# Performance work log

Hardware: AMD Instinct MI355X
Metric: run time of the kernel (lower is better)

Reference implementation:

```python
import jax, jax.numpy as jnp
import numpy as np

B, C, W, H, NH, FF, L = 4, 200, 300, 128, 8, 512, 2
PH = H // NH
MAXLEN = 200
PE_N = 512
NEG = -1e15


def _sinusoidal_pe():
    # fairseq-style sinusoidal table, get_embedding(512, hidden_size)
    half = H // 2
    freq = np.exp(np.arange(half, dtype=np.float64) * -(np.log(10000.0) / (half - 1)))
    ang = np.arange(PE_N, dtype=np.float64)[:, None] * freq[None, :]
    return jnp.asarray(np.concatenate([np.sin(ang), np.cos(ang)], axis=1), jnp.float32)

PE = _sinusoidal_pe()  # [512, H], frozen (requires_grad=False in torch)


def setup_inputs() -> dict:
    key = jax.random.key(0)
    ks = jax.random.split(key, 20)

    def lin(k, fan_in, shape):
        lim = 1.0 / np.sqrt(fan_in)
        return jax.random.uniform(k, shape, jnp.float32, -lim, lim)

    return {
        'chars': jax.random.normal(ks[0], (B, C, H), jnp.float32),
        'words': jax.random.normal(ks[1], (B, W, H), jnp.float32),
        'pos_s': jax.random.randint(ks[2], (B, C), 0, MAXLEN),
        'pos_e': jax.random.randint(ks[3], (B, C), 0, MAXLEN),
        'lex_s': jax.random.randint(ks[4], (B, W), 0, MAXLEN),
        'lex_e': jax.random.randint(ks[5], (B, W), 0, MAXLEN),
        'seq_len': jax.random.randint(ks[6], (B,), 100, C + 1),
        'lex_num': jax.random.randint(ks[7], (B,), 150, W + 1),
        # Four_Pos_Fusion 'ff': Linear(4H -> H) + ReLU
        'Wf': lin(ks[8], 4 * H, (4 * H, H)),
        'bf': jnp.zeros((H,), jnp.float32),
        # per-layer attention / FFN params, stacked on leading layer dim
        'Wq': lin(ks[9], H, (L, H, H)),  'bq': jnp.zeros((L, H), jnp.float32),
        'Wk': lin(ks[10], H, (L, H, H)), 'bk': jnp.zeros((L, H), jnp.float32),
        'Wv': lin(ks[11], H, (L, H, H)), 'bv': jnp.zeros((L, H), jnp.float32),
        'Wr': lin(ks[12], H, (L, H, H)), 'br': jnp.zeros((L, H), jnp.float32),
        'u_bias': jax.random.normal(ks[13], (L, NH, PH), jnp.float32) * 0.02,
        'v_bias': jax.random.normal(ks[14], (L, NH, PH), jnp.float32) * 0.02,
        'ln1_g': jnp.ones((L, H), jnp.float32), 'ln1_b': jnp.zeros((L, H), jnp.float32),
        'ln2_g': jnp.ones((L, H), jnp.float32), 'ln2_b': jnp.zeros((L, H), jnp.float32),
        'W1': lin(ks[15], H, (L, H, FF)),  'b1': jnp.zeros((L, FF), jnp.float32),
        'W2': lin(ks[16], FF, (L, FF, H)), 'b2': jnp.zeros((L, H), jnp.float32),
    }


def _ln(x, g, b):
    m = jnp.mean(x, -1, keepdims=True)
    v = jnp.var(x, -1, keepdims=True)
    return (x - m) / jnp.sqrt(v + 1e-5) * g + b


def reference(chars, words, pos_s, pos_e, lex_s, lex_e, seq_len, lex_num,
              Wf, bf, Wq, bq, Wk, bk, Wv, bv, Wr, br, u_bias, v_bias,
              ln1_g, ln1_b, ln2_g, ln2_b, W1, b1, W2, b2):
    # four relative-position distance tables (char span vs word span), offset by max_seq_len
    idx = lambda p, l: jnp.clip(p[:, :, None] - l[:, None, :] + MAXLEN, 0, PE_N - 1)
    # Linear(4H->H) over the concat of four gathered PE tensors, expressed as
    # a sum of 4 chunked matmuls to avoid materializing the [B,C,W,4H] concat.
    rel = (PE[idx(pos_s, lex_s)] @ Wf[0:H] + PE[idx(pos_s, lex_e)] @ Wf[H:2 * H]
           + PE[idx(pos_e, lex_s)] @ Wf[2 * H:3 * H] + PE[idx(pos_e, lex_e)] @ Wf[3 * H:4 * H] + bf)
    rel = jax.nn.relu(rel)  # [B, C, W, H]

    # char_lex_len_to_mask: valid (char i, word j) pairs
    mask = (jnp.arange(C) < seq_len[:, None])[:, :, None] & (jnp.arange(W) < lex_num[:, None])[:, None, :]
    mask = mask[:, None]  # [B, 1, C, W]

    out = chars
    for i in range(L):
        q = (out @ Wq[i] + bq[i]).reshape(B, C, NH, PH)
        k = (words @ Wk[i] + bk[i]).reshape(B, W, NH, PH)
        v = (words @ Wv[i] + bv[i]).reshape(B, W, NH, PH)
        r = (rel @ Wr[i] + br[i]).reshape(B, C, W, NH, PH)
        A_C = jnp.einsum('bcnp,bwnp->bncw', q + u_bias[i], k)
        B_D = jnp.einsum('bcnp,bcwnp->bncw', q + v_bias[i], r)
        score = jnp.where(mask, A_C + B_D, NEG)  # scale=False
        att = jax.nn.softmax(score, axis=-1)
        att = jnp.where(mask, att, 0.0)  # dropout=0 (eval)
        ctx = jnp.einsum('bncw,bwnp->bcnp', att, v).reshape(B, C, H)
        out = _ln(ctx + out, ln1_g[i], ln1_b[i])
        ff = jax.nn.relu(out @ W1[i] + b1[i]) @ W2[i] + b2[i]
        out = _ln(ff + out, ln2_g[i], ln2_b[i])
    return out
```

## Files before the change

kernel.cpp:

```cpp
#include <hip/hip_runtime.h>
#include <math.h>

#define B_ 4
#define C_ 200
#define CH_ 100
#define W_ 300
#define WP_ 304
#define H_ 128
#define NH_ 8
#define PH_ 16
#define FF_ 512
#define L_ 2
#define MAXLEN_ 200
#define PEN_ 512
#define WVS_ 136

typedef __bf16 bf16x8 __attribute__((ext_vector_type(8)));
typedef float f32x4v __attribute__((ext_vector_type(4)));

#define SEG_PEW   512
#define SEG_KV    (SEG_PEW + B_ * W_)
#define SEG_WR    (SEG_KV + 256)
#define SEG_W1T   (SEG_WR + 128)
#define PREP_BLOCKS (SEG_W1T + 128)

__global__ __launch_bounds__(128) void prep_kernel(
        const float* __restrict__ Wf, const float* __restrict__ bfv,
        const float* __restrict__ words,
        const float* __restrict__ Wk, const float* __restrict__ bk,
        const float* __restrict__ Wv, const float* __restrict__ bv,
        const float* __restrict__ Wr, const float* __restrict__ W1,
        const float* __restrict__ W2,
        __bf16* __restrict__ kb, __bf16* __restrict__ PEWb, __bf16* __restrict__ vTb,
        __bf16* __restrict__ WrB, __bf16* __restrict__ W1T, __bf16* __restrict__ W2T) {
    __shared__ __align__(16) float s_row[H_];
    __shared__ float s_tile[32][33];
    int t = threadIdx.x;
    if (blockIdx.x < SEG_PEW) {
        int p = blockIdx.x;
        {
            int j = (t < 64) ? t : (t - 64);
            double f = exp(-(double)j * (log(10000.0) / 63.0));
            double a = (double)p * f;
            s_row[t] = (float)((t < 64) ? sin(a) : cos(a));
        }
        __syncthreads();
        float acc0 = 0.f, acc1 = 0.f, acc2 = 0.f, acc3 = 0.f;
        for (int j = 0; j < H_; ++j) {
            float xv = s_row[j];
            int row = j * H_ + t;
            acc0 += xv * Wf[0 * H_ * H_ + row];
            acc1 += xv * Wf[1 * H_ * H_ + row];
            acc2 += xv * Wf[2 * H_ * H_ + row];
            acc3 += xv * Wf[3 * H_ * H_ + row];
        }
        PEWb[(0 * PEN_ + p) * H_ + t] = (__bf16)(acc0 + bfv[t]);
        PEWb[(1 * PEN_ + p) * H_ + t] = (__bf16)acc1;
        PEWb[(2 * PEN_ + p) * H_ + t] = (__bf16)acc2;
        PEWb[(3 * PEN_ + p) * H_ + t] = (__bf16)acc3;
    } else if (blockIdx.x < SEG_KV) {
        int rem = blockIdx.x - SEG_PEW;
        int bb = rem / W_, w = rem % W_;
        s_row[t] = words[rem * H_ + t];
        __syncthreads();
        const float4* row4 = (const float4*)s_row;
        #pragma unroll 1
        for (int li = 0; li < L_; ++li) {
            const float* wk = Wk + li * H_ * H_;
            const float* wv = Wv + li * H_ * H_;
            float4 ak = {0,0,0,0}, av = {0,0,0,0};
            #pragma unroll 2
            for (int g = 0; g < 32; ++g) {
                float4 x = row4[g];
                int j0 = 4 * g;
                ak.x += x.x * wk[(j0 + 0) * H_ + t];
                ak.y += x.y * wk[(j0 + 1) * H_ + t];
                ak.z += x.z * wk[(j0 + 2) * H_ + t];
                ak.w += x.w * wk[(j0 + 3) * H_ + t];
                av.x += x.x * wv[(j0 + 0) * H_ + t];
                av.y += x.y * wv[(j0 + 1) * H_ + t];
                av.z += x.z * wv[(j0 + 2) * H_ + t];
                av.w += x.w * wv[(j0 + 3) * H_ + t];
            }
            kb[(size_t)(li * B_ * W_ + rem) * H_ + t] =
                (__bf16)((ak.x + ak.y) + (ak.z + ak.w) + bk[li * H_ + t]);
            size_t vrow = ((size_t)(li * B_ + bb) * H_ + t) * WP_;
            vTb[vrow + w] = (__bf16)((av.x + av.y) + (av.z + av.w) + bv[li * H_ + t]);
            if (w == 0) {
                vTb[vrow + 300] = (__bf16)0.f; vTb[vrow + 301] = (__bf16)0.f;
                vTb[vrow + 302] = (__bf16)0.f; vTb[vrow + 303] = (__bf16)0.f;
            }
        }
    } else if (blockIdx.x < SEG_WR) {
        int i = (blockIdx.x - SEG_KV) * 128 + t;
        WrB[i] = (__bf16)Wr[i];
    } else if (blockIdx.x < SEG_W1T) {
        int blk = blockIdx.x - SEG_WR;
        int l = blk >> 6;
        int rem = blk & 63;
        int jt = rem >> 4;
        int ut = rem & 15;
        int r = t >> 5, cc = t & 31;
        #pragma unroll
        for (int k = 0; k < 8; ++k) {
            int j = jt * 32 + r + 4 * k;
            s_tile[r + 4 * k][cc] = W1[(l * H_ + j) * FF_ + ut * 32 + cc];
        }
        __syncthreads();
        int jl = t & 31, ul = t >> 5;
        #pragma unroll
        for (int k = 0; k < 8; ++k) {
            int u = ut * 32 + ul + 4 * k;
            W1T[((size_t)(l * FF_ + u)) * H_ + jt * 32 + jl] = (__bf16)s_tile[jl][ul + 4 * k];
        }
    } else {
        int blk = blockIdx.x - SEG_W1T;
        int l = blk >> 6;
        int rem = blk & 63;
        int ut = rem >> 2;
        int ht = rem & 3;
        int r = t >> 5, cc = t & 31;
        #pragma unroll
        for (int k = 0; k < 8; ++k) {
            int u = ut * 32 + r + 4 * k;
            s_tile[r + 4 * k][cc] = W2[(l * FF_ + u) * H_ + ht * 32 + cc];
        }
        __syncthreads();
        int ul = t & 31, hl = t >> 5;
        #pragma unroll
        for (int k = 0; k < 8; ++k) {
            int h = ht * 32 + hl + 4 * k;
            W2T[((size_t)(l * H_ + h)) * FF_ + ut * 32 + ul] = (__bf16)s_tile[ul][hl + 4 * k];
        }
    }
}

__global__ __launch_bounds__(256, 2) void mega_kernel(
    const float* __restrict__ chars,
    const int* __restrict__ pos_s, const int* __restrict__ pos_e,
    const int* __restrict__ lex_s, const int* __restrict__ lex_e,
    const int* __restrict__ seq_len, const int* __restrict__ lex_num,
    const float* __restrict__ Wq, const float* __restrict__ bq,
    const float* __restrict__ br,
    const float* __restrict__ u_bias, const float* __restrict__ v_bias,
    const float* __restrict__ ln1_g, const float* __restrict__ ln1_b,
    const float* __restrict__ ln2_g, const float* __restrict__ ln2_b,
    const float* __restrict__ b1, const float* __restrict__ b2,
    const __bf16* __restrict__ kb, const __bf16* __restrict__ PEWb,
    const __bf16* __restrict__ vTb, const __bf16* __restrict__ WrB,
    const __bf16* __restrict__ W1T, const __bf16* __restrict__ W2T,
    float* __restrict__ out) {

    __shared__ __align__(16) float s_x[2][H_], s_qv[2][H_];
    __shared__ __align__(16) __bf16 s_wvecb[2][16][WVS_];
    __shared__ __align__(16) __bf16 s_qub[2][16][WVS_];
    __shared__ float s_bterm[2][NH_];
    __shared__ __align__(16) float s_sc[2][NH_][WP_];
    __shared__ float s_red[2][132];
    __shared__ __align__(16) float s_hid[2][FF_];
    __shared__ float s_tmp[2][256];
    __shared__ int s_ls[W_], s_le[W_];

    int blk = blockIdx.x;
    int b = blk / CH_, c0 = blk % CH_;
    int t = threadIdx.x;
    int lane = t & 63;
    int wid = t >> 6;
    int l15 = lane & 15, quad = lane >> 4;

    if (t < H_) {
        s_x[0][t] = chars[(b * C_ + c0) * H_ + t];
        s_x[1][t] = chars[(b * C_ + c0 + CH_) * H_ + t];
    }
    for (int w = t; w < W_; w += 256) {
        s_ls[w] = lex_s[b * W_ + w];
        s_le[w] = lex_e[b * W_ + w];
    }
    for (int i = t; i < 2 * 8 * WVS_; i += 256) {
        int r = i / (8 * WVS_), rem = i % (8 * WVS_);
        s_wvecb[r][8 + rem / WVS_][rem % WVS_] = (__bf16)0.f;
    }
    for (int i = t; i < 2 * 16 * WVS_; i += 256) {
        int r = i / (16 * WVS_), rem = i % (16 * WVS_);
        s_qub[r][rem / WVS_][rem % WVS_] = (__bf16)0.f;
    }
    int ps0 = pos_s[b * C_ + c0],        pev0 = pos_e[b * C_ + c0];
    int ps1 = pos_s[b * C_ + c0 + CH_],  pev1 = pos_e[b * C_ + c0 + CH_];
    int slen = seq_len[b];
    int cvalid0 = (c0 < slen), cvalid1 = (c0 + CH_ < slen);
    int wnum = lex_num[b];
    __syncthreads();

    for (int li = 0; li < L_; ++li) {
        {
            int half = t >> 7, h = t & 127;
            const float* WqL = Wq + li * H_ * H_;
            const float4* x40 = (const float4*)s_x[0];
            const float4* x41 = (const float4*)s_x[1];
            float4 a0 = {0,0,0,0}, a1 = {0,0,0,0};
            #pragma unroll 2
            for (int g = half * 16; g < half * 16 + 16; ++g) {
                float4 xa = x40[g], xb = x41[g];
                int j0 = 4 * g;
                float w0 = WqL[(j0 + 0) * H_ + h], w1 = WqL[(j0 + 1) * H_ + h];
                float w2 = WqL[(j0 + 2) * H_ + h], w3 = WqL[(j0 + 3) * H_ + h];
                a0.x += xa.x * w0; a0.y += xa.y * w1; a0.z += xa.z * w2; a0.w += xa.w * w3;
                a1.x += xb.x * w0; a1.y += xb.y * w1; a1.z += xb.z * w2; a1.w += xb.w * w3;
            }
            s_tmp[0][t] = (a0.x + a0.y) + (a0.z + a0.w);
            s_tmp[1][t] = (a1.x + a1.y) + (a1.z + a1.w);
        }
        __syncthreads();
        if (t < H_) {
            #pragma unroll
            for (int r = 0; r < 2; ++r) {
                float acc = s_tmp[r][t] + s_tmp[r][t + 128] + bq[li * H_ + t];
                s_qub[r][t >> 4][t] = (__bf16)(acc + u_bias[li * H_ + t]);
                s_qv[r][t] = acc + v_bias[li * H_ + t];
            }
        }
        __syncthreads();

        if (t < H_) {
            const __bf16* WrRow = WrB + li * H_ * H_ + t * H_;
            #pragma unroll 2
            for (int n = 0; n < NH_; ++n) {
                bf16x8 w0 = *(const bf16x8*)(WrRow + n * PH_);
                bf16x8 w1 = *(const bf16x8*)(WrRow + n * PH_ + 8);
                #pragma unroll
                for (int r = 0; r < 2; ++r) {
                    const float4* qv4 = (const float4*)(s_qv[r] + n * PH_);
                    float4 q0 = qv4[0], q1 = qv4[1], q2 = qv4[2], q3 = qv4[3];
                    float4 a4;
                    a4.x = (float)w0[0] * q0.x + (float)w1[0] * q2.x;
                    a4.y = (float)w0[1] * q0.y + (float)w1[1] * q2.y;
                    a4.z = (float)w0[2] * q0.z + (float)w1[2] * q2.z;
                    a4.w = (float)w0[3] * q0.w + (float)w1[3] * q2.w;
                    a4.x += (float)w0[4] * q1.x + (float)w1[4] * q3.x;
                    a4.y += (float)w0[5] * q1.y + (float)w1[5] * q3.y;
                    a4.z += (float)w0[6] * q1.z + (float)w1[6] * q3.z;
                    a4.w += (float)w0[7] * q1.w + (float)w1[7] * q3.w;
                    s_wvecb[r][n][t] = (__bf16)((a4.x + a4.y) + (a4.z + a4.w));
                }
            }
        } else if (t < H_ + NH_) {
            int n = t - H_;
            const float4* br4 = (const float4*)(br + li * H_ + n * PH_);
            float4 b0 = br4[0], b1v = br4[1], b2v = br4[2], b3v = br4[3];
            #pragma unroll
            for (int r = 0; r < 2; ++r) {
                const float4* qv4 = (const float4*)(s_qv[r] + n * PH_);
                float4 q0 = qv4[0], q1 = qv4[1], q2 = qv4[2], q3 = qv4[3];
                float4 a4;
                a4.x = b0.x * q0.x + b2v.x * q2.x;
                a4.y = b0.y * q0.y + b2v.y * q2.y;
                a4.z = b0.z * q0.z + b2v.z * q2.z;
                a4.w = b0.w * q0.w + b2v.w * q2.w;
                a4.x += b1v.x * q1.x + b3v.x * q3.x;
                a4.y += b1v.y * q1.y + b3v.y * q3.y;
                a4.z += b1v.z * q1.z + b3v.z * q3.z;
                a4.w += b1v.w * q1.w + b3v.w * q3.w;
                s_bterm[r][n] = (a4.x + a4.y) + (a4.z + a4.w);
            }
        }
        __syncthreads();

        const __bf16* kL = kb + (size_t)(li * B_ + b) * W_ * H_;
        for (int tile = wid; tile < (W_ + 15) / 16; tile += 4) {
            int w0t = tile * 16;
            int w = w0t + l15; if (w > W_ - 1) w = W_ - 1;
            int ls = s_ls[w], le = s_le[w];
            int i00 = min(max(ps0 - ls + MAXLEN_, 0), PEN_ - 1);
            int i01 = min(max(ps0 - le + MAXLEN_, 0), PEN_ - 1);
            int i02 = min(max(pev0 - ls + MAXLEN_, 0), PEN_ - 1);
            int i03 = min(max(pev0 - le + MAXLEN_, 0), PEN_ - 1);
            int i10 = min(max(ps1 - ls + MAXLEN_, 0), PEN_ - 1);
            int i11 = min(max(ps1 - le + MAXLEN_, 0), PEN_ - 1);
            int i12 = min(max(pev1 - ls + MAXLEN_, 0), PEN_ - 1);
            int i13 = min(max(pev1 - le + MAXLEN_, 0), PEN_ - 1);
            const __bf16* r00 = PEWb + (size_t)(0 * PEN_ + i00) * H_;
            const __bf16* r01 = PEWb + (size_t)(1 * PEN_ + i01) * H_;
            const __bf16* r02 = PEWb + (size_t)(2 * PEN_ + i02) * H_;
            const __bf16* r03 = PEWb + (size_t)(3 * PEN_ + i03) * H_;
            const __bf16* r10 = PEWb + (size_t)(0 * PEN_ + i10) * H_;
            const __bf16* r11 = PEWb + (size_t)(1 * PEN_ + i11) * H_;
            const __bf16* r12 = PEWb + (size_t)(2 * PEN_ + i12) * H_;
            const __bf16* r13 = PEWb + (size_t)(3 * PEN_ + i13) * H_;
            const __bf16* kr = kL + (size_t)w * H_;
            const __bf16* wrow0 = &s_wvecb[0][l15][0];
            const __bf16* wrow1 = &s_wvecb[1][l15][0];
            const __bf16* qrow0 = &s_qub[0][l15][0];
            const __bf16* qrow1 = &s_qub[1][l15][0];
            f32x4v acc0 = {0.f,0.f,0.f,0.f}, acc1 = {0.f,0.f,0.f,0.f};
            #pragma unroll 1
            for (int s = 0; s < 4; ++s) {
                int h0 = s * 32 + quad * 8;
                bf16x8 K = *(const bf16x8*)(kr + h0);
                {
                    bf16x8 t0 = *(const bf16x8*)(r00 + h0);
                    bf16x8 t1 = *(const bf16x8*)(r01 + h0);
                    bf16x8 t2 = *(const bf16x8*)(r02 + h0);
                    bf16x8 t3 = *(const bf16x8*)(r03 + h0);
                    bf16x8 A;
                    #pragma unroll
                    for (int j = 0; j < 8; ++j)
                        A[j] = (__bf16)fmaxf((float)t0[j] + (float)t1[j] + (float)t2[j] + (float)t3[j], 0.f);
                    bf16x8 Bf = *(const bf16x8*)(wrow0 + h0);
                    acc0 = __builtin_amdgcn_mfma_f32_16x16x32_bf16(A, Bf, acc0, 0, 0, 0);
                    bf16x8 Bq = *(const bf16x8*)(qrow0 + h0);
                    acc0 = __builtin_amdgcn_mfma_f32_16x16x32_bf16(K, Bq, acc0, 0, 0, 0);
                }
                {
                    bf16x8 t0 = *(const bf16x8*)(r10 + h0);
                    bf16x8 t1 = *(const bf16x8*)(r11 + h0);
                    bf16x8 t2 = *(const bf16x8*)(r12 + h0);
                    bf16x8 t3 = *(const bf16x8*)(r13 + h0);
                    bf16x8 A;
                    #pragma unroll
                    for (int j = 0; j < 8; ++j)
                        A[j] = (__bf16)fmaxf((float)t0[j] + (float)t1[j] + (float)t2[j] + (float)t3[j], 0.f);
                    bf16x8 Bf = *(const bf16x8*)(wrow1 + h0);
                    acc1 = __builtin_amdgcn_mfma_f32_16x16x32_bf16(A, Bf, acc1, 0, 0, 0);
                    bf16x8 Bq = *(const bf16x8*)(qrow1 + h0);
                    acc1 = __builtin_amdgcn_mfma_f32_16x16x32_bf16(K, Bq, acc1, 0, 0, 0);
                }
            }
            if (l15 < NH_) {
                float bt0 = s_bterm[0][l15], bt1 = s_bterm[1][l15];
                #pragma unroll
                for (int r = 0; r < 4; ++r) {
                    int wr = w0t + quad * 4 + r;
                    if (wr < W_) {
                        s_sc[0][l15][wr] = acc0[r] + bt0;
                        s_sc[1][l15][wr] = acc1[r] + bt1;
                    }
                }
            }
        }
        __syncthreads();

        {
            int n = t >> 5, ln_ = t & 31;
            #pragma unroll
            for (int r = 0; r < 2; ++r) {
                int cval = r ? cvalid1 : cvalid0;
                if (cval) {
                    float m = -INFINITY;
                    for (int w = ln_; w < wnum; w += 32) m = fmaxf(m, s_sc[r][n][w]);
                    #pragma unroll
                    for (int off = 16; off > 0; off >>= 1) m = fmaxf(m, __shfl_xor(m, off, 32));
                    float sum = 0.f;
                    for (int w = ln_; w < wnum; w += 32) sum += expf(s_sc[r][n][w] - m);
                    #pragma unroll
                    for (int off = 16; off > 0; off >>= 1) sum += __shfl_xor(sum, off, 32);
                    float inv = 1.f / sum;
                    for (int w = ln_; w < WP_; w += 32)
                        s_sc[r][n][w] = (w < wnum) ? expf(s_sc[r][n][w] - m) * inv : 0.f;
                } else {
                    for (int w = ln_; w < WP_; w += 32) s_sc[r][n][w] = 0.f;
                }
            }
        }
        __syncthreads();

        {
            int h = t & 127, half = t >> 7, n = h >> 4;
            const __bf16* vrow = vTb + ((size_t)(li * B_ + b) * H_ + h) * WP_;
            const float4* att0 = (const float4*)(s_sc[0][n]);
            const float4* att1 = (const float4*)(s_sc[1][n]);
            float4 a0 = {0,0,0,0}, a1 = {0,0,0,0};
            #pragma unroll 2
            for (int g = half * 19; g < half * 19 + 19; ++g) {
                bf16x8 vv = *(const bf16x8*)(vrow + 8 * g);
                float4 p00 = att0[2 * g], p01 = att0[2 * g + 1];
                float4 p10 = att1[2 * g], p11 = att1[2 * g + 1];
                float v0 = (float)vv[0], v1 = (float)vv[1], v2 = (float)vv[2], v3 = (float)vv[3];
                float v4 = (float)vv[4], v5 = (float)vv[5], v6 = (float)vv[6], v7 = (float)vv[7];
                a0.x += p00.x * v0 + p01.x * v4;
                a0.y += p00.y * v1 + p01.y * v5;
                a0.z += p00.z * v2 + p01.z * v6;
                a0.w += p00.w * v3 + p01.w * v7;
                a1.x += p10.x * v0 + p11.x * v4;
                a1.y += p10.y * v1 + p11.y * v5;
                a1.z += p10.z * v2 + p11.z * v6;
                a1.w += p10.w * v3 + p11.w * v7;
            }
            s_tmp[0][t] = (a0.x + a0.y) + (a0.z + a0.w);
            s_tmp[1][t] = (a1.x + a1.y) + (a1.z + a1.w);
        }
        __syncthreads();

        if (t < 128) {
            s_red[0][t] = s_tmp[0][t] + s_tmp[0][t + 128] + s_x[0][t];
        } else {
            int e = t - 128;
            s_red[1][e] = s_tmp[1][e] + s_tmp[1][e + 128] + s_x[1][e];
        }
        __syncthreads();
        if (t < 128) {
            int r = t >> 6, l = t & 63;
            float a = s_red[r][l], bb = s_red[r][l + 64];
            float s = a + bb, ss = a * a + bb * bb;
            #pragma unroll
            for (int off = 32; off > 0; off >>= 1) {
                s += __shfl_down(s, off);
                ss += __shfl_down(ss, off);
            }
            if (l == 0) {
                float mean = s * (1.f / 128.f);
                float var = ss * (1.f / 128.f) - mean * mean;
                s_red[r][128] = mean;
                s_red[r][129] = rsqrtf(var + 1e-5f);
            }
        }
        __syncthreads();
        if (t < H_) {
            float g1 = ln1_g[li * H_ + t], b1v = ln1_b[li * H_ + t];
            #pragma unroll
            for (int r = 0; r < 2; ++r)
                s_x[r][t] = (s_red[r][t] - s_red[r][128]) * s_red[r][129] * g1 + b1v;
        }
        __syncthreads();

        {
            const __bf16* W1l = W1T + (size_t)li * FF_ * H_;
            int u0 = t * 2;
            const __bf16* ra = W1l + (size_t)u0 * H_;
            const __bf16* rb = W1l + (size_t)(u0 + 1) * H_;
            const float4* x40 = (const float4*)s_x[0];
            const float4* x41 = (const float4*)s_x[1];
            float4 a00 = {0,0,0,0}, a01 = {0,0,0,0}, a10 = {0,0,0,0}, a11 = {0,0,0,0};
            #pragma unroll 2
            for (int g = 0; g < 16; ++g) {
                bf16x8 wa = *(const bf16x8*)(ra + 8 * g);
                bf16x8 wb = *(const bf16x8*)(rb + 8 * g);
                float4 xa0 = x40[2 * g], xa1 = x40[2 * g + 1];
                float4 xb0 = x41[2 * g], xb1 = x41[2 * g + 1];
                a00.x += xa0.x * (float)wa[0] + xa1.x * (float)wa[4];
                a00.y += xa0.y * (float)wa[1] + xa1.y * (float)wa[5];
                a00.z += xa0.z * (float)wa[2] + xa1.z * (float)wa[6];
                a00.w += xa0.w * (float)wa[3] + xa1.w * (float)wa[7];
                a01.x += xa0.x * (float)wb[0] + xa1.x * (float)wb[4];
                a01.y += xa0.y * (float)wb[1] + xa1.y * (float)wb[5];
                a01.z += xa0.z * (float)wb[2] + xa1.z * (float)wb[6];
                a01.w += xa0.w * (float)wb[3] + xa1.w * (float)wb[7];
                a10.x += xb0.x * (float)wa[0] + xb1.x * (float)wa[4];
                a10.y += xb0.y * (float)wa[1] + xb1.y * (float)wa[5];
                a10.z += xb0.z * (float)wa[2] + xb1.z * (float)wa[6];
                a10.w += xb0.w * (float)wa[3] + xb1.w * (float)wa[7];
                a11.x += xb0.x * (float)wb[0] + xb1.x * (float)wb[4];
                a11.y += xb0.y * (float)wb[1] + xb1.y * (float)wb[5];
                a11.z += xb0.z * (float)wb[2] + xb1.z * (float)wb[6];
                a11.w += xb0.w * (float)wb[3] + xb1.w * (float)wb[7];
            }
            float bb0 = b1[li * FF_ + u0], bb1 = b1[li * FF_ + u0 + 1];
            s_hid[0][u0]     = fmaxf((a00.x + a00.y) + (a00.z + a00.w) + bb0, 0.f);
            s_hid[0][u0 + 1] = fmaxf((a01.x + a01.y) + (a01.z + a01.w) + bb1, 0.f);
            s_hid[1][u0]     = fmaxf((a10.x + a10.y) + (a10.z + a10.w) + bb0, 0.f);
            s_hid[1][u0 + 1] = fmaxf((a11.x + a11.y) + (a11.z + a11.w) + bb1, 0.f);
        }
        __syncthreads();

        {
            int half = t >> 7, h = t & 127;
            const __bf16* wrow2 = W2T + ((size_t)li * H_ + h) * FF_ + half * 256;
            const float4* h40 = (const float4*)(s_hid[0] + half * 256);
            const float4* h41 = (const float4*)(s_hid[1] + half * 256);
            float4 a0 = {0,0,0,0}, a1 = {0,0,0,0};
            #pragma unroll 2
            for (int g = 0; g < 32; ++g) {
                bf16x8 wv = *(const bf16x8*)(wrow2 + 8 * g);
                float4 p00 = h40[2 * g], p01 = h40[2 * g + 1];
                float4 p10 = h41[2 * g], p11 = h41[2 * g + 1];
                float v0 = (float)wv[0], v1 = (float)wv[1], v2 = (float)wv[2], v3 = (float)wv[3];
                float v4 = (float)wv[4], v5 = (float)wv[5], v6 = (float)wv[6], v7 = (float)wv[7];
                a0.x += p00.x * v0 + p01.x * v4;
                a0.y += p00.y * v1 + p01.y * v5;
                a0.z += p00.z * v2 + p01.z * v6;
                a0.w += p00.w * v3 + p01.w * v7;
                a1.x += p10.x * v0 + p11.x * v4;
                a1.y += p10.y * v1 + p11.y * v5;
                a1.z += p10.z * v2 + p11.z * v6;
                a1.w += p10.w * v3 + p11.w * v7;
            }
            s_tmp[0][t] = (a0.x + a0.y) + (a0.z + a0.w);
            s_tmp[1][t] = (a1.x + a1.y) + (a1.z + a1.w);
        }
        __syncthreads();

        if (t < 128) {
            s_red[0][t] = s_tmp[0][t] + s_tmp[0][t + 128] + b2[li * H_ + t] + s_x[0][t];
        } else {
            int e = t - 128;
            s_red[1][e] = s_tmp[1][e] + s_tmp[1][e + 128] + b2[li * H_ + e] + s_x[1][e];
        }
        __syncthreads();
        if (t < 128) {
            int r = t >> 6, l = t & 63;
            float a = s_red[r][l], bb = s_red[r][l + 64];
            float s = a + bb, ss = a * a + bb * bb;
            #pragma unroll
            for (int off = 32; off > 0; off >>= 1) {
                s += __shfl_down(s, off);
                ss += __shfl_down(ss, off);
            }
            if (l == 0) {
                float mean = s * (1.f / 128.f);
                float var = ss * (1.f / 128.f) - mean * mean;
                s_red[r][128] = mean;
                s_red[r][129] = rsqrtf(var + 1e-5f);
            }
        }
        __syncthreads();
        if (t < H_) {
            float g2 = ln2_g[li * H_ + t], b2v = ln2_b[li * H_ + t];
            #pragma unroll
            for (int r = 0; r < 2; ++r)
                s_x[r][t] = (s_red[r][t] - s_red[r][128]) * s_red[r][129] * g2 + b2v;
        }
        __syncthreads();
    }

    if (t < H_) {
        out[(b * C_ + c0) * H_ + t] = s_x[0][t];
        out[(b * C_ + c0 + CH_) * H_ + t] = s_x[1][t];
    }
}

extern "C" void kernel_launch(void* const* d_in, const int* in_sizes, int n_in,
                              void* d_out, int out_size, void* d_ws, size_t ws_size,
                              hipStream_t stream) {
    const float* chars  = (const float*)d_in[0];
    const float* words  = (const float*)d_in[1];
    const int* pos_s   = (const int*)d_in[2];
    const int* pos_e   = (const int*)d_in[3];
    const int* lex_s   = (const int*)d_in[4];
    const int* lex_e   = (const int*)d_in[5];
    const int* seq_len = (const int*)d_in[6];
    const int* lex_num = (const int*)d_in[7];
    const float* Wf  = (const float*)d_in[8];
    const float* bfv = (const float*)d_in[9];
    const float* Wq  = (const float*)d_in[10];
    const float* bq  = (const float*)d_in[11];
    const float* Wk  = (const float*)d_in[12];
    const float* bk  = (const float*)d_in[13];
    const float* Wv  = (const float*)d_in[14];
    const float* bv  = (const float*)d_in[15];
    const float* Wr  = (const float*)d_in[16];
    const float* br  = (const float*)d_in[17];
    const float* u_bias = (const float*)d_in[18];
    const float* v_bias = (const float*)d_in[19];
    const float* ln1_g  = (const float*)d_in[20];
    const float* ln1_b  = (const float*)d_in[21];
    const float* ln2_g  = (const float*)d_in[22];
    const float* ln2_b  = (const float*)d_in[23];
    const float* W1  = (const float*)d_in[24];
    const float* b1  = (const float*)d_in[25];
    const float* W2  = (const float*)d_in[26];
    const float* b2  = (const float*)d_in[27];

    __bf16* kb   = (__bf16*)d_ws;
    __bf16* PEWb = kb + (size_t)L_ * B_ * W_ * H_;
    __bf16* vTb  = PEWb + 4 * PEN_ * H_;
    __bf16* WrB  = vTb + (size_t)L_ * B_ * H_ * WP_;
    __bf16* W1T  = WrB + L_ * H_ * H_;
    __bf16* W2T  = W1T + L_ * H_ * FF_;

    prep_kernel<<<dim3(PREP_BLOCKS), dim3(128), 0, stream>>>(
        Wf, bfv, words, Wk, bk, Wv, bv, Wr, W1, W2,
        kb, PEWb, vTb, WrB, W1T, W2T);

    mega_kernel<<<dim3(B_ * CH_), dim3(256), 0, stream>>>(
        chars, pos_s, pos_e, lex_s, lex_e, seq_len, lex_num,
        Wq, bq, br, u_bias, v_bias,
        ln1_g, ln1_b, ln2_g, ln2_b, b1, b2,
        kb, PEWb, vTb, WrB, W1T, W2T, (float*)d_out);
}
```

Measured before the change: 267.7 us.

## Cache relative-position A fragments in registers across layers

The gathered and ReLU'd positional fusion fragments (A0/A1) are computed once in layer 0 and kept in registers (5x4 bf16x8 per row pair), then reused in layer 1 instead of re-gathering four PE rows and summing again. The layer and tile loops are fully unrolled so the cached arrays can stay in registers. This removes half of the scattered global PE gathers and the conversion arithmetic, but adds up to 160 VGPRs per thread, which risks spills or lower occupancy.

```diff
diff --git a/kernel.cpp b/kernel.cpp
--- a/kernel.cpp
+++ b/kernel.cpp
@@ -14,6 +14,7 @@
 #define MAXLEN_ 200
 #define PEN_ 512
 #define WVS_ 136
+#define NTILE_ 19
 
 typedef __bf16 bf16x8 __attribute__((ext_vector_type(8)));
 typedef float f32x4v __attribute__((ext_vector_type(4)));
@@ -191,6 +192,9 @@
     int wnum = lex_num[b];
     __syncthreads();
 
+    bf16x8 Ac0[5][4], Ac1[5][4];
+
+    #pragma unroll
     for (int li = 0; li < L_; ++li) {
         {
             int half = t >> 7, h = t & 127;
@@ -266,73 +270,98 @@
         __syncthreads();
 
         const __bf16* kL = kb + (size_t)(li * B_ + b) * W_ * H_;
-        for (int tile = wid; tile < (W_ + 15) / 16; tile += 4) {
-            int w0t = tile * 16;
-            int w = w0t + l15; if (w > W_ - 1) w = W_ - 1;
-            int ls = s_ls[w], le = s_le[w];
-            int i00 = min(max(ps0 - ls + MAXLEN_, 0), PEN_ - 1);
-            int i01 = min(max(ps0 - le + MAXLEN_, 0), PEN_ - 1);
-            int i02 = min(max(pev0 - ls + MAXLEN_, 0), PEN_ - 1);
-            int i03 = min(max(pev0 - le + MAXLEN_, 0), PEN_ - 1);
-            int i10 = min(max(ps1 - ls + MAXLEN_, 0), PEN_ - 1);
-            int i11 = min(max(ps1 - le + MAXLEN_, 0), PEN_ - 1);
-            int i12 = min(max(pev1 - ls + MAXLEN_, 0), PEN_ - 1);
-            int i13 = min(max(pev1 - le + MAXLEN_, 0), PEN_ - 1);
-            const __bf16* r00 = PEWb + (size_t)(0 * PEN_ + i00) * H_;
-            const __bf16* r01 = PEWb + (size_t)(1 * PEN_ + i01) * H_;
-            const __bf16* r02 = PEWb + (size_t)(2 * PEN_ + i02) * H_;
-            const __bf16* r03 = PEWb + (size_t)(3 * PEN_ + i03) * H_;
-            const __bf16* r10 = PEWb + (size_t)(0 * PEN_ + i10) * H_;
-            const __bf16* r11 = PEWb + (size_t)(1 * PEN_ + i11) * H_;
-            const __bf16* r12 = PEWb + (size_t)(2 * PEN_ + i12) * H_;
-            const __bf16* r13 = PEWb + (size_t)(3 * PEN_ + i13) * H_;
-            const __bf16* kr = kL + (size_t)w * H_;
+        {
             const __bf16* wrow0 = &s_wvecb[0][l15][0];
             const __bf16* wrow1 = &s_wvecb[1][l15][0];
             const __bf16* qrow0 = &s_qub[0][l15][0];
             const __bf16* qrow1 = &s_qub[1][l15][0];
-            f32x4v acc0 = {0.f,0.f,0.f,0.f}, acc1 = {0.f,0.f,0.f,0.f};
-            #pragma unroll 1
-            for (int s = 0; s < 4; ++s) {
-                int h0 = s * 32 + quad * 8;
-                bf16x8 K = *(const bf16x8*)(kr + h0);
-                {
-                    bf16x8 t0 = *(const bf16x8*)(r00 + h0);
-                    bf16x8 t1 = *(const bf16x8*)(r01 + h0);
-                    bf16x8 t2 = *(const bf16x8*)(r02 + h0);
-                    bf16x8 t3 = *(const bf16x8*)(r03 + h0);
-                    bf16x8 A;
-                    #pragma unroll
-                    for (int j = 0; j < 8; ++j)
-                        A[j] = (__bf16)fmaxf((float)t0[j] + (float)t1[j] + (float)t2[j] + (float)t3[j], 0.f);
-                    bf16x8 Bf = *(const bf16x8*)(wrow0 + h0);
-                    acc0 = __builtin_amdgcn_mfma_f32_16x16x32_bf16(A, Bf, acc0, 0, 0, 0);
-                    bf16x8 Bq = *(const bf16x8*)(qrow0 + h0);
-                    acc0 = __builtin_amdgcn_mfma_f32_16x16x32_bf16(K, Bq, acc0, 0, 0, 0);
-                }
-                {
-                    bf16x8 t0 = *(const bf16x8*)(r10 + h0);
-                    bf16x8 t1 = *(const bf16x8*)(r11 + h0);
-                    bf16x8 t2 = *(const bf16x8*)(r12 + h0);
-                    bf16x8 t3 = *(const bf16x8*)(r13 + h0);
-                    bf16x8 A;
-                    #pragma unroll
-                    for (int j = 0; j < 8; ++j)
-                        A[j] = (__bf16)fmaxf((float)t0[j] + (float)t1[j] + (float)t2[j] + (float)t3[j], 0.f);
-                    bf16x8 Bf = *(const bf16x8*)(wrow1 + h0);
-                    acc1 = __builtin_amdgcn_mfma_f32_16x16x32_bf16(A, Bf, acc1, 0, 0, 0);
-                    bf16x8 Bq = *(const bf16x8*)(qrow1 + h0);
-                    acc1 = __builtin_amdgcn_mfma_f32_16x16x32_bf16(K, Bq, acc1, 0, 0, 0);
-                }
-            }
-            if (l15 < NH_) {
-                float bt0 = s_bterm[0][l15], bt1 = s_bterm[1][l15];
-                #pragma unroll
-                for (int r = 0; r < 4; ++r) {
-                    int wr = w0t + quad * 4 + r;
-                    if (wr < W_) {
-                        s_sc[0][l15][wr] = acc0[r] + bt0;
-                        s_sc[1][l15][wr] = acc1[r] + bt1;
+            #pragma unroll
+            for (int tc = 0; tc < 5; ++tc) {
+                int tile = wid + 4 * tc;
+                if (tile < NTILE_) {
+                    int w0t = tile * 16;
+                    int w = w0t + l15; if (w > W_ - 1) w = W_ - 1;
+                    const __bf16* kr = kL + (size_t)w * H_;
+                    f32x4v acc0 = {0.f,0.f,0.f,0.f}, acc1 = {0.f,0.f,0.f,0.f};
+                    if (li == 0) {
+                        int ls = s_ls[w], le = s_le[w];
+                        int i00 = min(max(ps0 - ls + MAXLEN_, 0), PEN_ - 1);
+                        int i01 = min(max(ps0 - le + MAXLEN_, 0), PEN_ - 1);
+                        int i02 = min(max(pev0 - ls + MAXLEN_, 0), PEN_ - 1);
+                        int i03 = min(max(pev0 - le + MAXLEN_, 0), PEN_ - 1);
+                        int i10 = min(max(ps1 - ls + MAXLEN_, 0), PEN_ - 1);
+                        int i11 = min(max(ps1 - le + MAXLEN_, 0), PEN_ - 1);
+                        int i12 = min(max(pev1 - ls + MAXLEN_, 0), PEN_ - 1);
+                        int i13 = min(max(pev1 - le + MAXLEN_, 0), PEN_ - 1);
+                        const __bf16* r00 = PEWb + (size_t)(0 * PEN_ + i00) * H_;
+                        const __bf16* r01 = PEWb + (size_t)(1 * PEN_ + i01) * H_;
+                        const __bf16* r02 = PEWb + (size_t)(2 * PEN_ + i02) * H_;
+                        const __bf16* r03 = PEWb + (size_t)(3 * PEN_ + i03) * H_;
+                        const __bf16* r10 = PEWb + (size_t)(0 * PEN_ + i10) * H_;
+                        const __bf16* r11 = PEWb + (size_t)(1 * PEN_ + i11) * H_;
+                        const __bf16* r12 = PEWb + (size_t)(2 * PEN_ + i12) * H_;
+                        const __bf16* r13 = PEWb + (size_t)(3 * PEN_ + i13) * H_;
+                        #pragma unroll
+                        for (int s = 0; s < 4; ++s) {
+                            int h0 = s * 32 + quad * 8;
+                            bf16x8 K = *(const bf16x8*)(kr + h0);
+                            bf16x8 A0, A1;
+                            {
+                                bf16x8 t0 = *(const bf16x8*)(r00 + h0);
+                                bf16x8 t1 = *(const bf16x8*)(r01 + h0);
+                                bf16x8 t2 = *(const bf16x8*)(r02 + h0);
+                                bf16x8 t3 = *(const bf16x8*)(r03 + h0);
+                                #pragma unroll
+                                for (int j = 0; j < 8; ++j)
+                                    A0[j] = (__bf16)fmaxf((float)t0[j] + (float)t1[j] + (float)t2[j] + (float)t3[j], 0.f);
+                            }
+                            {
+                                bf16x8 t0 = *(const bf16x8*)(r10 + h0);
+                                bf16x8 t1 = *(const bf16x8*)(r11 + h0);
+                                bf16x8 t2 = *(const bf16x8*)(r12 + h0);
+                                bf16x8 t3 = *(const bf16x8*)(r13 + h0);
+                                #pragma unroll
+                                for (int j = 0; j < 8; ++j)
+                                    A1[j] = (__bf16)fmaxf((float)t0[j] + (float)t1[j] + (float)t2[j] + (float)t3[j], 0.f);
+                            }
+                            Ac0[tc][s] = A0;
+                            Ac1[tc][s] = A1;
+                            bf16x8 Bf0 = *(const bf16x8*)(wrow0 + h0);
+                            acc0 = __builtin_amdgcn_mfma_f32_16x16x32_bf16(A0, Bf0, acc0, 0, 0, 0);
+                            bf16x8 Bq0 = *(const bf16x8*)(qrow0 + h0);
+                            acc0 = __builtin_amdgcn_mfma_f32_16x16x32_bf16(K, Bq0, acc0, 0, 0, 0);
+                            bf16x8 Bf1 = *(const bf16x8*)(wrow1 + h0);
+                            acc1 = __builtin_amdgcn_mfma_f32_16x16x32_bf16(A1, Bf1, acc1, 0, 0, 0);
+                            bf16x8 Bq1 = *(const bf16x8*)(qrow1 + h0);
+                            acc1 = __builtin_amdgcn_mfma_f32_16x16x32_bf16(K, Bq1, acc1, 0, 0, 0);
+                        }
+                    } else {
+                        #pragma unroll
+                        for (int s = 0; s < 4; ++s) {
+                            int h0 = s * 32 + quad * 8;
+                            bf16x8 K = *(const bf16x8*)(kr + h0);
+                            bf16x8 A0 = Ac0[tc][s];
+                            bf16x8 A1 = Ac1[tc][s];
+                            bf16x8 Bf0 = *(const bf16x8*)(wrow0 + h0);
+                            acc0 = __builtin_amdgcn_mfma_f32_16x16x32_bf16(A0, Bf0, acc0, 0, 0, 0);
+                            bf16x8 Bq0 = *(const bf16x8*)(qrow0 + h0);
+                            acc0 = __builtin_amdgcn_mfma_f32_16x16x32_bf16(K, Bq0, acc0, 0, 0, 0);
+                            bf16x8 Bf1 = *(const bf16x8*)(wrow1 + h0);
+                            acc1 = __builtin_amdgcn_mfma_f32_16x16x32_bf16(A1, Bf1, acc1, 0, 0, 0);
+                            bf16x8 Bq1 = *(const bf16x8*)(qrow1 + h0);
+                            acc1 = __builtin_amdgcn_mfma_f32_16x16x32_bf16(K, Bq1, acc1, 0, 0, 0);
+                        }
+                    }
+                    if (l15 < NH_) {
+                        float bt0 = s_bterm[0][l15], bt1 = s_bterm[1][l15];
+                        #pragma unroll
+                        for (int r = 0; r < 4; ++r) {
+                            int wr = w0t + quad * 4 + r;
+                            if (wr < W_) {
+                                s_sc[0][l15][wr] = acc0[r] + bt0;
+                                s_sc[1][l15][wr] = acc1[r] + bt1;
+                            }
+                        }
                     }
                 }
             }
```

New measurement: 240.6 us (median of 2 runs). -10.1%, faster.
